# Performance work log

Hardware: AMD Instinct MI355X
Metric: run time of the kernel (lower is better)

## Reference

```python
import jax, jax.numpy as jnp
import numpy as np

HIDDEN = 2048
INTER = 1408
N_ROUTED = 32
N_SHARED = 2
TOP_K = 6
B, S = 2, 1024


def setup_inputs() -> dict:
    key = jax.random.key(0)
    ks = jax.random.split(key, 9)
    scale = 0.02
    x = jax.random.normal(ks[0], (B, S, HIDDEN), dtype=jnp.float32)
    w_router = jax.random.normal(ks[1], (HIDDEN, N_ROUTED), dtype=jnp.float32) * scale
    wg = jax.random.normal(ks[2], (N_ROUTED, HIDDEN, INTER), dtype=jnp.float32) * scale
    wu = jax.random.normal(ks[3], (N_ROUTED, HIDDEN, INTER), dtype=jnp.float32) * scale
    wd = jax.random.normal(ks[4], (N_ROUTED, INTER, HIDDEN), dtype=jnp.float32) * scale
    sg = jax.random.normal(ks[5], (N_SHARED, HIDDEN, INTER), dtype=jnp.float32) * scale
    su = jax.random.normal(ks[6], (N_SHARED, HIDDEN, INTER), dtype=jnp.float32) * scale
    sd = jax.random.normal(ks[7], (N_SHARED, INTER, HIDDEN), dtype=jnp.float32) * scale
    return {"x": x, "w_router": w_router, "wg": wg, "wu": wu, "wd": wd,
            "sg": sg, "su": su, "sd": sd}


def _swiglu(xf, wg_e, wu_e, wd_e):
    # xf: [T, D]; wg_e/wu_e: [D, F]; wd_e: [F, D]
    h = jax.nn.silu(xf @ wg_e) * (xf @ wu_e)
    return h @ wd_e


def reference(x, w_router, wg, wu, wd, sg, su, sd):
    Bb, Ss, D = x.shape
    xf = x.reshape(-1, D)                      # [T, D], T = B*S
    T = xf.shape[0]

    # Shared experts: applied densely to every token, summed.
    shared = jnp.zeros_like(xf)
    for i in range(sg.shape[0]):               # small fixed count (2)
        shared = shared + _swiglu(xf, sg[i], su[i], sd[i])

    # Router: softmax over all routed experts, then top-k + renormalize.
    probs = jax.nn.softmax(xf @ w_router, axis=-1)            # [T, E]
    topw, topi = jax.lax.top_k(probs, TOP_K)                  # [T, K]
    topw = topw / jnp.sum(topw, axis=-1, keepdims=True)

    # Dense [T, E] combine weights (zero where expert not selected).
    E = wg.shape[0]
    wdense = jnp.zeros((T, E), dtype=xf.dtype)
    wdense = wdense.at[jnp.arange(T)[:, None], topi].add(topw)

    # Scan over experts, accumulating weighted expert outputs (memory-light).
    def body(acc, ew):
        wg_e, wu_e, wd_e, w_e = ew            # w_e: [T] combine weight for this expert
        y = _swiglu(xf, wg_e, wu_e, wd_e)     # [T, D]
        return acc + w_e[:, None] * y, None

    routed, _ = jax.lax.scan(body, jnp.zeros_like(xf), (wg, wu, wd, wdense.T))

    return (shared + routed).reshape(Bb, Ss, D)
```

## Files before the change

kernel.cpp:

```cpp
#include <hip/hip_runtime.h>
#include <hip/hip_bf16.h>

#define T_TOK 2048
#define D_HID 2048
#define F_INT 1408
#define N_EXP 32
#define TOPK 6
#define NJOBS 34
#define SH_BASE 12288
#define ROWS_TOTAL 16384
#define MAXT_GU 288
#define MAXT_DN 159
#define LDSW 40

typedef __bf16 bf16;
typedef __bf16 bf16x4 __attribute__((ext_vector_type(4)));
typedef __bf16 bf16x8 __attribute__((ext_vector_type(8)));
typedef float f32x4 __attribute__((ext_vector_type(4)));

#define BAR() asm volatile("s_waitcnt lgkmcnt(0)\n\ts_barrier" ::: "memory")

__device__ __forceinline__ int swz(int r, int k) {
    return r * LDSW + (((k >> 2) ^ ((r >> 2) & 7)) << 2) + (k & 3);
}

__device__ __forceinline__ int decode_tile(const int* __restrict__ counts, int bid,
                                           int NBN, int MSH, int NSH,
                                           int& job, int& n0, int& m0) {
    int total = 0;
    for (int j = 0; j < NJOBS; ++j) {
        int c = (j < N_EXP) ? counts[j] : T_TOK;
        total += ((c + (1 << MSH) - 1) >> MSH) * NBN;
    }
    if (bid >= total) return 0;
    int q = total >> 3, r = total & 7, x = bid & 7, o = bid >> 3;
    int L = (x < r ? x * (q + 1) : r * (q + 1) + (x - r) * q) + o;
    int acc = 0;
    for (int j = 0; j < NJOBS; ++j) {
        int c = (j < N_EXP) ? counts[j] : T_TOK;
        int tc = (c + (1 << MSH) - 1) >> MSH;
        int b = tc * NBN;
        if (L < acc + b) {
            int rem = L - acc;
            int n0i = rem / tc;
            job = j;
            n0 = n0i << NSH;
            m0 = (rem - n0i * tc) << MSH;
            return 1;
        }
        acc += b;
    }
    return 0;
}

__global__ __launch_bounds__(256) void k_router(const float* __restrict__ x,
                                                const float* __restrict__ wr,
                                                int* __restrict__ counts,
                                                int* __restrict__ tok_e,
                                                float* __restrict__ tok_w) {
    int t = blockIdx.x;
    int tid = threadIdx.x;
    __shared__ float xs[D_HID];
    __shared__ float part[8][32];
    __shared__ float probs[N_EXP];

    const float4* xsrc = (const float4*)(x + (size_t)t * D_HID);
    float4* xdst = (float4*)xs;
    for (int i = tid; i < D_HID / 4; i += 256) xdst[i] = xsrc[i];
    __syncthreads();

    int e = tid & 31, c = tid >> 5;
    float p = 0.f;
    const float* wp = wr + e;
    #pragma unroll 8
    for (int h = c * 256; h < c * 256 + 256; ++h) p += xs[h] * wp[h * 32];
    part[c][e] = p;
    __syncthreads();

    if (tid < 32) {
        float l = 0.f;
        #pragma unroll
        for (int cc = 0; cc < 8; ++cc) l += part[cc][tid];
        float m = l;
        for (int off = 16; off; off >>= 1) m = fmaxf(m, __shfl_xor(m, off));
        float ex = __expf(l - m);
        float s = ex;
        for (int off = 16; off; off >>= 1) s += __shfl_xor(s, off);
        probs[tid] = ex / s;
    }
    __syncthreads();

    if (tid == 0) {
        unsigned used = 0;
        int ids[TOPK]; float wsv[TOPK]; float wsum = 0.f;
        for (int k = 0; k < TOPK; ++k) {
            int best = 0; float bv = -1.f;
            for (int ee = 0; ee < N_EXP; ++ee)
                if (!((used >> ee) & 1u) && probs[ee] > bv) { bv = probs[ee]; best = ee; }
            used |= 1u << best;
            ids[k] = best; wsv[k] = bv; wsum += bv;
        }
        float inv = 1.f / wsum;
        for (int k = 0; k < TOPK; ++k) {
            tok_e[t * TOPK + k] = ids[k];
            tok_w[t * TOPK + k] = wsv[k] * inv;
            atomicAdd(&counts[ids[k]], 1);
        }
    }
}

__global__ void k_plan(const int* __restrict__ counts, int* __restrict__ offs,
                       int* __restrict__ cursors) {
    int tid = threadIdx.x;
    if (tid < N_EXP) cursors[tid] = 0;
    if (tid == 0) {
        int o = 0;
        offs[0] = 0;
        for (int e2 = 0; e2 < N_EXP; ++e2) { o += counts[e2]; offs[e2 + 1] = o; }
        offs[33] = offs[32] + T_TOK;
        offs[34] = offs[33] + T_TOK;
    }
}

__global__ __launch_bounds__(256) void k_assign(const int* __restrict__ tok_e,
                                                const int* __restrict__ offs,
                                                int* __restrict__ cursors,
                                                int* __restrict__ slots,
                                                int* __restrict__ rowtok) {
    int t = blockIdx.x * 256 + threadIdx.x;
    #pragma unroll
    for (int k = 0; k < TOPK; ++k) {
        int e = tok_e[t * TOPK + k];
        int pos = atomicAdd(&cursors[e], 1);
        int slot = offs[e] + pos;
        slots[t * TOPK + k] = slot;
        rowtok[slot] = t;
    }
    rowtok[SH_BASE + t] = t;
    rowtok[SH_BASE + T_TOK + t] = t;
}

__global__ __launch_bounds__(256, 3) void k_gateup(
    const float* __restrict__ x, const float* __restrict__ wg, const float* __restrict__ wu,
    const float* __restrict__ sg, const float* __restrict__ su,
    const int* __restrict__ rowtok, const int* __restrict__ counts, const int* __restrict__ offs,
    bf16* __restrict__ H) {

    int job, n0, m0;
    if (!decode_tile(counts, blockIdx.x, F_INT / 128, 6, 7, job, n0, m0)) return;
    int cnt = (job < N_EXP) ? counts[job] : T_TOK;
    int base = offs[job];
    const float* Wg = (job < N_EXP) ? wg + (size_t)job * D_HID * F_INT
                                    : sg + (size_t)(job - N_EXP) * D_HID * F_INT;
    const float* Wu = (job < N_EXP) ? wu + (size_t)job * D_HID * F_INT
                                    : su + (size_t)(job - N_EXP) * D_HID * F_INT;

    __shared__ bf16 As[2][64 * LDSW];
    __shared__ bf16 Bg[2][128 * LDSW];
    __shared__ bf16 Bu[2][128 * LDSW];

    int tid = threadIdx.x;
    int lane = tid & 63;
    int wid = tid >> 6;
    int wm = (wid >> 1) * 32;
    int wn = (wid & 1) * 64;

    int ar = tid >> 2;
    int akh = (tid & 3) * 8;
    int grow_a = m0 + ar; if (grow_a > cnt - 1) grow_a = cnt - 1;
    const float* asrc = x + (size_t)rowtok[base + grow_a] * D_HID + akh;

    int k4 = (tid >> 5) * 4;
    int nn = (tid & 31) * 4;
    const float* gsrc = Wg + (size_t)k4 * F_INT + n0 + nn;
    const float* usrc = Wu + (size_t)k4 * F_INT + n0 + nn;

    f32x4 accg[2][4], accu[2][4];
    f32x4 zero = {0.f, 0.f, 0.f, 0.f};
    #pragma unroll
    for (int i = 0; i < 2; ++i)
        #pragma unroll
        for (int j = 0; j < 4; ++j) { accg[i][j] = zero; accu[i][j] = zero; }

    float4 a_r[2], g_r[4], u_r[4];

    auto LOAD = [&](int k0) {
        const float4* s4 = (const float4*)(asrc + k0);
        a_r[0] = s4[0]; a_r[1] = s4[1];
        const float* g0 = gsrc + (size_t)k0 * F_INT;
        g_r[0] = *(const float4*)g0;
        g_r[1] = *(const float4*)(g0 + F_INT);
        g_r[2] = *(const float4*)(g0 + 2 * F_INT);
        g_r[3] = *(const float4*)(g0 + 3 * F_INT);
        const float* u0 = usrc + (size_t)k0 * F_INT;
        u_r[0] = *(const float4*)u0;
        u_r[1] = *(const float4*)(u0 + F_INT);
        u_r[2] = *(const float4*)(u0 + 2 * F_INT);
        u_r[3] = *(const float4*)(u0 + 3 * F_INT);
    };

    auto WRITE = [&](int s) {
        #pragma unroll
        for (int q = 0; q < 2; ++q) {
            float4 f = a_r[q];
            bf16x4 v = {(bf16)f.x, (bf16)f.y, (bf16)f.z, (bf16)f.w};
            *(bf16x4*)&As[s][swz(ar, akh + 4 * q)] = v;
        }
        bf16x4 p0 = {(bf16)g_r[0].x, (bf16)g_r[1].x, (bf16)g_r[2].x, (bf16)g_r[3].x};
        bf16x4 p1 = {(bf16)g_r[0].y, (bf16)g_r[1].y, (bf16)g_r[2].y, (bf16)g_r[3].y};
        bf16x4 p2 = {(bf16)g_r[0].z, (bf16)g_r[1].z, (bf16)g_r[2].z, (bf16)g_r[3].z};
        bf16x4 p3 = {(bf16)g_r[0].w, (bf16)g_r[1].w, (bf16)g_r[2].w, (bf16)g_r[3].w};
        *(bf16x4*)&Bg[s][swz(nn + 0, k4)] = p0;
        *(bf16x4*)&Bg[s][swz(nn + 1, k4)] = p1;
        *(bf16x4*)&Bg[s][swz(nn + 2, k4)] = p2;
        *(bf16x4*)&Bg[s][swz(nn + 3, k4)] = p3;
        bf16x4 q0 = {(bf16)u_r[0].x, (bf16)u_r[1].x, (bf16)u_r[2].x, (bf16)u_r[3].x};
        bf16x4 q1 = {(bf16)u_r[0].y, (bf16)u_r[1].y, (bf16)u_r[2].y, (bf16)u_r[3].y};
        bf16x4 q2 = {(bf16)u_r[0].z, (bf16)u_r[1].z, (bf16)u_r[2].z, (bf16)u_r[3].z};
        bf16x4 q3 = {(bf16)u_r[0].w, (bf16)u_r[1].w, (bf16)u_r[2].w, (bf16)u_r[3].w};
        *(bf16x4*)&Bu[s][swz(nn + 0, k4)] = q0;
        *(bf16x4*)&Bu[s][swz(nn + 1, k4)] = q1;
        *(bf16x4*)&Bu[s][swz(nn + 2, k4)] = q2;
        *(bf16x4*)&Bu[s][swz(nn + 3, k4)] = q3;
    };

    const int NT = D_HID / 32;
    LOAD(0);
    WRITE(0);
    LOAD(32);
    BAR();

    for (int kt = 0; kt < NT; ++kt) {
        int cur = kt & 1;
        if (kt + 1 < NT) WRITE(cur ^ 1);
        if (kt + 2 < NT) LOAD((kt + 2) * 32);

        int kk = (lane >> 4) * 8;
        bf16x8 af[2];
        #pragma unroll
        for (int mf = 0; mf < 2; ++mf) {
            int R = wm + mf * 16 + (lane & 15);
            bf16x4 lo = *(const bf16x4*)&As[cur][swz(R, kk)];
            bf16x4 hi = *(const bf16x4*)&As[cur][swz(R, kk + 4)];
            af[mf] = __builtin_shufflevector(lo, hi, 0, 1, 2, 3, 4, 5, 6, 7);
        }
        #pragma unroll
        for (int nf = 0; nf < 4; ++nf) {
            int rn = wn + nf * 16 + (lane & 15);
            int o0 = swz(rn, kk), o1 = swz(rn, kk + 4);
            bf16x4 bl = *(const bf16x4*)&Bg[cur][o0];
            bf16x4 bh = *(const bf16x4*)&Bg[cur][o1];
            bf16x8 bfr = __builtin_shufflevector(bl, bh, 0, 1, 2, 3, 4, 5, 6, 7);
            bf16x4 ul = *(const bf16x4*)&Bu[cur][o0];
            bf16x4 uh = *(const bf16x4*)&Bu[cur][o1];
            bf16x8 ufr = __builtin_shufflevector(ul, uh, 0, 1, 2, 3, 4, 5, 6, 7);
            #pragma unroll
            for (int mf = 0; mf < 2; ++mf) {
                accg[mf][nf] = __builtin_amdgcn_mfma_f32_16x16x32_bf16(af[mf], bfr, accg[mf][nf], 0, 0, 0);
                accu[mf][nf] = __builtin_amdgcn_mfma_f32_16x16x32_bf16(af[mf], ufr, accu[mf][nf], 0, 0, 0);
            }
        }
        BAR();
    }

    #pragma unroll
    for (int mf = 0; mf < 2; ++mf) {
        #pragma unroll
        for (int nf = 0; nf < 4; ++nf) {
            int col = n0 + wn + nf * 16 + (lane & 15);
            #pragma unroll
            for (int r = 0; r < 4; ++r) {
                int grow = m0 + wm + mf * 16 + (lane >> 4) * 4 + r;
                if (grow < cnt) {
                    float g = accg[mf][nf][r];
                    float u = accu[mf][nf][r];
                    float h = g * u / (1.f + __expf(-g));
                    H[(size_t)(base + grow) * F_INT + col] = (bf16)h;
                }
            }
        }
    }
}

__global__ __launch_bounds__(256, 3) void k_down(
    const bf16* __restrict__ H, const float* __restrict__ wd, const float* __restrict__ sd,
    const int* __restrict__ counts, const int* __restrict__ offs,
    bf16* __restrict__ P) {

    int job, n0, m0;
    if (!decode_tile(counts, blockIdx.x, D_HID / 128, 7, 7, job, n0, m0)) return;
    int cnt = (job < N_EXP) ? counts[job] : T_TOK;
    int base = offs[job];
    const float* Wd = (job < N_EXP) ? wd + (size_t)job * F_INT * D_HID
                                    : sd + (size_t)(job - N_EXP) * F_INT * D_HID;

    __shared__ bf16 As[2][128 * LDSW];
    __shared__ bf16 Bs[2][128 * LDSW];

    int tid = threadIdx.x;
    int lane = tid & 63;
    int wid = tid >> 6;
    int wm = (wid >> 1) * 64;
    int wn = (wid & 1) * 64;

    int ar = tid >> 1;
    int akh = (tid & 1) * 16;
    int grow_a = m0 + ar; if (grow_a > cnt - 1) grow_a = cnt - 1;
    const bf16* asrc = H + (size_t)(base + grow_a) * F_INT + akh;

    int k4 = (tid >> 5) * 4;
    int nn = (tid & 31) * 4;
    const float* bsrc = Wd + (size_t)k4 * D_HID + n0 + nn;

    f32x4 acc[4][4];
    f32x4 zero = {0.f, 0.f, 0.f, 0.f};
    #pragma unroll
    for (int i = 0; i < 4; ++i)
        #pragma unroll
        for (int j = 0; j < 4; ++j) acc[i][j] = zero;

    bf16x8 h_r[2];
    float4 b_r[4];

    auto LOAD = [&](int k0) {
        h_r[0] = *(const bf16x8*)(asrc + k0);
        h_r[1] = *(const bf16x8*)(asrc + k0 + 8);
        const float* b0 = bsrc + (size_t)k0 * D_HID;
        b_r[0] = *(const float4*)b0;
        b_r[1] = *(const float4*)(b0 + D_HID);
        b_r[2] = *(const float4*)(b0 + 2 * D_HID);
        b_r[3] = *(const float4*)(b0 + 3 * D_HID);
    };

    auto WRITE = [&](int s) {
        bf16x4 w0 = __builtin_shufflevector(h_r[0], h_r[0], 0, 1, 2, 3);
        bf16x4 w1 = __builtin_shufflevector(h_r[0], h_r[0], 4, 5, 6, 7);
        bf16x4 w2 = __builtin_shufflevector(h_r[1], h_r[1], 0, 1, 2, 3);
        bf16x4 w3 = __builtin_shufflevector(h_r[1], h_r[1], 4, 5, 6, 7);
        *(bf16x4*)&As[s][swz(ar, akh + 0)]  = w0;
        *(bf16x4*)&As[s][swz(ar, akh + 4)]  = w1;
        *(bf16x4*)&As[s][swz(ar, akh + 8)]  = w2;
        *(bf16x4*)&As[s][swz(ar, akh + 12)] = w3;
        bf16x4 p0 = {(bf16)b_r[0].x, (bf16)b_r[1].x, (bf16)b_r[2].x, (bf16)b_r[3].x};
        bf16x4 p1 = {(bf16)b_r[0].y, (bf16)b_r[1].y, (bf16)b_r[2].y, (bf16)b_r[3].y};
        bf16x4 p2 = {(bf16)b_r[0].z, (bf16)b_r[1].z, (bf16)b_r[2].z, (bf16)b_r[3].z};
        bf16x4 p3 = {(bf16)b_r[0].w, (bf16)b_r[1].w, (bf16)b_r[2].w, (bf16)b_r[3].w};
        *(bf16x4*)&Bs[s][swz(nn + 0, k4)] = p0;
        *(bf16x4*)&Bs[s][swz(nn + 1, k4)] = p1;
        *(bf16x4*)&Bs[s][swz(nn + 2, k4)] = p2;
        *(bf16x4*)&Bs[s][swz(nn + 3, k4)] = p3;
    };

    const int NT = F_INT / 32;
    LOAD(0);
    WRITE(0);
    LOAD(32);
    BAR();

    for (int kt = 0; kt < NT; ++kt) {
        int cur = kt & 1;
        if (kt + 1 < NT) WRITE(cur ^ 1);
        if (kt + 2 < NT) LOAD((kt + 2) * 32);

        int kk = (lane >> 4) * 8;
        bf16x8 af[4];
        #pragma unroll
        for (int mf = 0; mf < 4; ++mf) {
            int R = wm + mf * 16 + (lane & 15);
            bf16x4 lo = *(const bf16x4*)&As[cur][swz(R, kk)];
            bf16x4 hi = *(const bf16x4*)&As[cur][swz(R, kk + 4)];
            af[mf] = __builtin_shufflevector(lo, hi, 0, 1, 2, 3, 4, 5, 6, 7);
        }
        #pragma unroll
        for (int nf = 0; nf < 4; ++nf) {
            int rn = wn + nf * 16 + (lane & 15);
            bf16x4 bl = *(const bf16x4*)&Bs[cur][swz(rn, kk)];
            bf16x4 bh = *(const bf16x4*)&Bs[cur][swz(rn, kk + 4)];
            bf16x8 bfr = __builtin_shufflevector(bl, bh, 0, 1, 2, 3, 4, 5, 6, 7);
            #pragma unroll
            for (int mf = 0; mf < 4; ++mf)
                acc[mf][nf] = __builtin_amdgcn_mfma_f32_16x16x32_bf16(af[mf], bfr, acc[mf][nf], 0, 0, 0);
        }
        BAR();
    }

    #pragma unroll
    for (int mf = 0; mf < 4; ++mf) {
        #pragma unroll
        for (int nf = 0; nf < 4; ++nf) {
            int col = n0 + wn + nf * 16 + (lane & 15);
            #pragma unroll
            for (int r = 0; r < 4; ++r) {
                int grow = m0 + wm + mf * 16 + (lane >> 4) * 4 + r;
                if (grow < cnt)
                    P[(size_t)(base + grow) * D_HID + col] = (bf16)acc[mf][nf][r];
            }
        }
    }
}

__global__ __launch_bounds__(256) void k_combine(const bf16* __restrict__ P,
                                                 const int* __restrict__ slots,
                                                 const float* __restrict__ tok_w,
                                                 float* __restrict__ out) {
    int t = blockIdx.x;
    int tid = threadIdx.x;
    __shared__ int ss[TOPK];
    __shared__ float ww[TOPK];
    if (tid < TOPK) { ss[tid] = slots[t * TOPK + tid]; ww[tid] = tok_w[t * TOPK + tid]; }
    __syncthreads();
    int c0 = tid * 8;
    float acc[8];
    {
        bf16x8 v0 = *(const bf16x8*)(P + (size_t)(SH_BASE + t) * D_HID + c0);
        bf16x8 v1 = *(const bf16x8*)(P + (size_t)(SH_BASE + T_TOK + t) * D_HID + c0);
        #pragma unroll
        for (int i = 0; i < 8; ++i) acc[i] = (float)v0[i] + (float)v1[i];
    }
    #pragma unroll
    for (int k = 0; k < TOPK; ++k) {
        bf16x8 v = *(const bf16x8*)(P + (size_t)ss[k] * D_HID + c0);
        float w = ww[k];
        #pragma unroll
        for (int i = 0; i < 8; ++i) acc[i] += w * (float)v[i];
    }
    float4 o0 = {acc[0], acc[1], acc[2], acc[3]};
    float4 o1 = {acc[4], acc[5], acc[6], acc[7]};
    *(float4*)(out + (size_t)t * D_HID + c0) = o0;
    *(float4*)(out + (size_t)t * D_HID + c0 + 4) = o1;
}

extern "C" void kernel_launch(void* const* d_in, const int* in_sizes, int n_in,
                              void* d_out, int out_size, void* d_ws, size_t ws_size,
                              hipStream_t stream) {
    const float* x  = (const float*)d_in[0];
    const float* wr = (const float*)d_in[1];
    const float* wg = (const float*)d_in[2];
    const float* wu = (const float*)d_in[3];
    const float* wd = (const float*)d_in[4];
    const float* sg = (const float*)d_in[5];
    const float* su = (const float*)d_in[6];
    const float* sd = (const float*)d_in[7];
    float* out = (float*)d_out;

    char* w = (char*)d_ws;
    int*   counts   = (int*)(w + 0);
    int*   cursors  = (int*)(w + 256);
    int*   offs     = (int*)(w + 512);
    int*   tok_e    = (int*)(w + 8192);
    float* tok_w    = (float*)(w + 8192 + 49152);
    int*   slots    = (int*)(w + 8192 + 2 * 49152);
    int*   rowtok   = (int*)(w + 8192 + 3 * 49152);
    bf16*  H        = (bf16*)(w + 262144);
    bf16*  P        = (bf16*)(w + 262144 + (size_t)ROWS_TOTAL * F_INT * 2);

    hipMemsetAsync(counts, 0, 128, stream);
    k_router<<<T_TOK, 256, 0, stream>>>(x, wr, counts, tok_e, tok_w);
    k_plan<<<1, 64, 0, stream>>>(counts, offs, cursors);
    k_assign<<<T_TOK / 256, 256, 0, stream>>>(tok_e, offs, cursors, slots, rowtok);
    k_gateup<<<MAXT_GU * (F_INT / 128), 256, 0, stream>>>(
        x, wg, wu, sg, su, rowtok, counts, offs, H);
    k_down<<<MAXT_DN * (D_HID / 128), 256, 0, stream>>>(
        H, wd, sd, counts, offs, P);
    k_combine<<<T_TOK, 256, 0, stream>>>(P, slots, tok_w, out);
}
```

Measured before the change: 811.4 us.

## Pre-convert activations to bf16 and use 16-byte LDS swizzle for fragment loads

Adds a kernel that converts x to bf16 once, so the gate/up GEMM gathers half as many activation bytes and skips the per-tile float-to-bf16 conversion. The LDS swizzle moves from 4-element to 8-element granularity, so A and B fragments are read with a single 16-byte LDS load instead of two 8-byte loads and a shuffle. This costs an extra launch plus an extra write and read of the converted activations, and the new swizzle may change bank-conflict behaviour for the 4-element transposed B-tile stores.

```diff
diff --git a/kernel.cpp b/kernel.cpp
--- a/kernel.cpp
+++ b/kernel.cpp
@@ -20,8 +20,8 @@
 
 #define BAR() asm volatile("s_waitcnt lgkmcnt(0)\n\ts_barrier" ::: "memory")
 
-__device__ __forceinline__ int swz(int r, int k) {
-    return r * LDSW + (((k >> 2) ^ ((r >> 2) & 7)) << 2) + (k & 3);
+__device__ __forceinline__ int swz16(int r, int k) {
+    return r * LDSW + (((k >> 3) ^ ((r >> 3) & 3)) << 3) + (k & 7);
 }
 
 __device__ __forceinline__ int decode_tile(const int* __restrict__ counts, int bid,
@@ -53,6 +53,16 @@
     return 0;
 }
 
+__global__ __launch_bounds__(256) void k_xcvt(const float* __restrict__ x,
+                                              bf16* __restrict__ xb) {
+    int i = blockIdx.x * 2048 + threadIdx.x * 8;
+    float4 f0 = *(const float4*)(x + i);
+    float4 f1 = *(const float4*)(x + i + 4);
+    bf16x8 v = {(bf16)f0.x, (bf16)f0.y, (bf16)f0.z, (bf16)f0.w,
+                (bf16)f1.x, (bf16)f1.y, (bf16)f1.z, (bf16)f1.w};
+    *(bf16x8*)(xb + i) = v;
+}
+
 __global__ __launch_bounds__(256) void k_router(const float* __restrict__ x,
                                                 const float* __restrict__ wr,
                                                 int* __restrict__ counts,
@@ -141,7 +151,7 @@
 }
 
 __global__ __launch_bounds__(256, 3) void k_gateup(
-    const float* __restrict__ x, const float* __restrict__ wg, const float* __restrict__ wu,
+    const bf16* __restrict__ xb, const float* __restrict__ wg, const float* __restrict__ wu,
     const float* __restrict__ sg, const float* __restrict__ su,
     const int* __restrict__ rowtok, const int* __restrict__ counts, const int* __restrict__ offs,
     bf16* __restrict__ H) {
@@ -166,9 +176,9 @@
     int wn = (wid & 1) * 64;
 
     int ar = tid >> 2;
-    int akh = (tid & 3) * 8;
+    int akg = tid & 3;
     int grow_a = m0 + ar; if (grow_a > cnt - 1) grow_a = cnt - 1;
-    const float* asrc = x + (size_t)rowtok[base + grow_a] * D_HID + akh;
+    const bf16* asrc = xb + (size_t)rowtok[base + grow_a] * D_HID + akg * 8;
 
     int k4 = (tid >> 5) * 4;
     int nn = (tid & 31) * 4;
@@ -182,11 +192,11 @@
         #pragma unroll
         for (int j = 0; j < 4; ++j) { accg[i][j] = zero; accu[i][j] = zero; }
 
-    float4 a_r[2], g_r[4], u_r[4];
+    bf16x8 a_r8;
+    float4 g_r[4], u_r[4];
 
     auto LOAD = [&](int k0) {
-        const float4* s4 = (const float4*)(asrc + k0);
-        a_r[0] = s4[0]; a_r[1] = s4[1];
+        a_r8 = *(const bf16x8*)(asrc + k0);
         const float* g0 = gsrc + (size_t)k0 * F_INT;
         g_r[0] = *(const float4*)g0;
         g_r[1] = *(const float4*)(g0 + F_INT);
@@ -200,28 +210,23 @@
     };
 
     auto WRITE = [&](int s) {
-        #pragma unroll
-        for (int q = 0; q < 2; ++q) {
-            float4 f = a_r[q];
-            bf16x4 v = {(bf16)f.x, (bf16)f.y, (bf16)f.z, (bf16)f.w};
-            *(bf16x4*)&As[s][swz(ar, akh + 4 * q)] = v;
-        }
+        *(bf16x8*)&As[s][swz16(ar, akg * 8)] = a_r8;
         bf16x4 p0 = {(bf16)g_r[0].x, (bf16)g_r[1].x, (bf16)g_r[2].x, (bf16)g_r[3].x};
         bf16x4 p1 = {(bf16)g_r[0].y, (bf16)g_r[1].y, (bf16)g_r[2].y, (bf16)g_r[3].y};
         bf16x4 p2 = {(bf16)g_r[0].z, (bf16)g_r[1].z, (bf16)g_r[2].z, (bf16)g_r[3].z};
         bf16x4 p3 = {(bf16)g_r[0].w, (bf16)g_r[1].w, (bf16)g_r[2].w, (bf16)g_r[3].w};
-        *(bf16x4*)&Bg[s][swz(nn + 0, k4)] = p0;
-        *(bf16x4*)&Bg[s][swz(nn + 1, k4)] = p1;
-        *(bf16x4*)&Bg[s][swz(nn + 2, k4)] = p2;
-        *(bf16x4*)&Bg[s][swz(nn + 3, k4)] = p3;
+        *(bf16x4*)&Bg[s][swz16(nn + 0, k4)] = p0;
+        *(bf16x4*)&Bg[s][swz16(nn + 1, k4)] = p1;
+        *(bf16x4*)&Bg[s][swz16(nn + 2, k4)] = p2;
+        *(bf16x4*)&Bg[s][swz16(nn + 3, k4)] = p3;
         bf16x4 q0 = {(bf16)u_r[0].x, (bf16)u_r[1].x, (bf16)u_r[2].x, (bf16)u_r[3].x};
         bf16x4 q1 = {(bf16)u_r[0].y, (bf16)u_r[1].y, (bf16)u_r[2].y, (bf16)u_r[3].y};
         bf16x4 q2 = {(bf16)u_r[0].z, (bf16)u_r[1].z, (bf16)u_r[2].z, (bf16)u_r[3].z};
         bf16x4 q3 = {(bf16)u_r[0].w, (bf16)u_r[1].w, (bf16)u_r[2].w, (bf16)u_r[3].w};
-        *(bf16x4*)&Bu[s][swz(nn + 0, k4)] = q0;
-        *(bf16x4*)&Bu[s][swz(nn + 1, k4)] = q1;
-        *(bf16x4*)&Bu[s][swz(nn + 2, k4)] = q2;
-        *(bf16x4*)&Bu[s][swz(nn + 3, k4)] = q3;
+        *(bf16x4*)&Bu[s][swz16(nn + 0, k4)] = q0;
+        *(bf16x4*)&Bu[s][swz16(nn + 1, k4)] = q1;
+        *(bf16x4*)&Bu[s][swz16(nn + 2, k4)] = q2;
+        *(bf16x4*)&Bu[s][swz16(nn + 3, k4)] = q3;
     };
 
     const int NT = D_HID / 32;
@@ -235,25 +240,16 @@
         if (kt + 1 < NT) WRITE(cur ^ 1);
         if (kt + 2 < NT) LOAD((kt + 2) * 32);
 
-        int kk = (lane >> 4) * 8;
+        int kgl = (lane >> 4) * 8;
         bf16x8 af[2];
         #pragma unroll
-        for (int mf = 0; mf < 2; ++mf) {
-            int R = wm + mf * 16 + (lane & 15);
-            bf16x4 lo = *(const bf16x4*)&As[cur][swz(R, kk)];
-            bf16x4 hi = *(const bf16x4*)&As[cur][swz(R, kk + 4)];
-            af[mf] = __builtin_shufflevector(lo, hi, 0, 1, 2, 3, 4, 5, 6, 7);
-        }
+        for (int mf = 0; mf < 2; ++mf)
+            af[mf] = *(const bf16x8*)&As[cur][swz16(wm + mf * 16 + (lane & 15), kgl)];
         #pragma unroll
         for (int nf = 0; nf < 4; ++nf) {
             int rn = wn + nf * 16 + (lane & 15);
-            int o0 = swz(rn, kk), o1 = swz(rn, kk + 4);
-            bf16x4 bl = *(const bf16x4*)&Bg[cur][o0];
-            bf16x4 bh = *(const bf16x4*)&Bg[cur][o1];
-            bf16x8 bfr = __builtin_shufflevector(bl, bh, 0, 1, 2, 3, 4, 5, 6, 7);
-            bf16x4 ul = *(const bf16x4*)&Bu[cur][o0];
-            bf16x4 uh = *(const bf16x4*)&Bu[cur][o1];
-            bf16x8 ufr = __builtin_shufflevector(ul, uh, 0, 1, 2, 3, 4, 5, 6, 7);
+            bf16x8 bfr = *(const bf16x8*)&Bg[cur][swz16(rn, kgl)];
+            bf16x8 ufr = *(const bf16x8*)&Bu[cur][swz16(rn, kgl)];
             #pragma unroll
             for (int mf = 0; mf < 2; ++mf) {
                 accg[mf][nf] = __builtin_amdgcn_mfma_f32_16x16x32_bf16(af[mf], bfr, accg[mf][nf], 0, 0, 0);
@@ -304,9 +300,9 @@
     int wn = (wid & 1) * 64;
 
     int ar = tid >> 1;
-    int akh = (tid & 1) * 16;
+    int akg2 = (tid & 1) * 2;
     int grow_a = m0 + ar; if (grow_a > cnt - 1) grow_a = cnt - 1;
-    const bf16* asrc = H + (size_t)(base + grow_a) * F_INT + akh;
+    const bf16* asrc = H + (size_t)(base + grow_a) * F_INT + akg2 * 8;
 
     int k4 = (tid >> 5) * 4;
     int nn = (tid & 31) * 4;
@@ -333,22 +329,16 @@
     };
 
     auto WRITE = [&](int s) {
-        bf16x4 w0 = __builtin_shufflevector(h_r[0], h_r[0], 0, 1, 2, 3);
-        bf16x4 w1 = __builtin_shufflevector(h_r[0], h_r[0], 4, 5, 6, 7);
-        bf16x4 w2 = __builtin_shufflevector(h_r[1], h_r[1], 0, 1, 2, 3);
-        bf16x4 w3 = __builtin_shufflevector(h_r[1], h_r[1], 4, 5, 6, 7);
-        *(bf16x4*)&As[s][swz(ar, akh + 0)]  = w0;
-        *(bf16x4*)&As[s][swz(ar, akh + 4)]  = w1;
-        *(bf16x4*)&As[s][swz(ar, akh + 8)]  = w2;
-        *(bf16x4*)&As[s][swz(ar, akh + 12)] = w3;
+        *(bf16x8*)&As[s][swz16(ar, akg2 * 8)] = h_r[0];
+        *(bf16x8*)&As[s][swz16(ar, (akg2 + 1) * 8)] = h_r[1];
         bf16x4 p0 = {(bf16)b_r[0].x, (bf16)b_r[1].x, (bf16)b_r[2].x, (bf16)b_r[3].x};
         bf16x4 p1 = {(bf16)b_r[0].y, (bf16)b_r[1].y, (bf16)b_r[2].y, (bf16)b_r[3].y};
         bf16x4 p2 = {(bf16)b_r[0].z, (bf16)b_r[1].z, (bf16)b_r[2].z, (bf16)b_r[3].z};
         bf16x4 p3 = {(bf16)b_r[0].w, (bf16)b_r[1].w, (bf16)b_r[2].w, (bf16)b_r[3].w};
-        *(bf16x4*)&Bs[s][swz(nn + 0, k4)] = p0;
-        *(bf16x4*)&Bs[s][swz(nn + 1, k4)] = p1;
-        *(bf16x4*)&Bs[s][swz(nn + 2, k4)] = p2;
-        *(bf16x4*)&Bs[s][swz(nn + 3, k4)] = p3;
+        *(bf16x4*)&Bs[s][swz16(nn + 0, k4)] = p0;
+        *(bf16x4*)&Bs[s][swz16(nn + 1, k4)] = p1;
+        *(bf16x4*)&Bs[s][swz16(nn + 2, k4)] = p2;
+        *(bf16x4*)&Bs[s][swz16(nn + 3, k4)] = p3;
     };
 
     const int NT = F_INT / 32;
@@ -362,21 +352,15 @@
         if (kt + 1 < NT) WRITE(cur ^ 1);
         if (kt + 2 < NT) LOAD((kt + 2) * 32);
 
-        int kk = (lane >> 4) * 8;
+        int kgl = (lane >> 4) * 8;
         bf16x8 af[4];
         #pragma unroll
-        for (int mf = 0; mf < 4; ++mf) {
-            int R = wm + mf * 16 + (lane & 15);
-            bf16x4 lo = *(const bf16x4*)&As[cur][swz(R, kk)];
-            bf16x4 hi = *(const bf16x4*)&As[cur][swz(R, kk + 4)];
-            af[mf] = __builtin_shufflevector(lo, hi, 0, 1, 2, 3, 4, 5, 6, 7);
-        }
+        for (int mf = 0; mf < 4; ++mf)
+            af[mf] = *(const bf16x8*)&As[cur][swz16(wm + mf * 16 + (lane & 15), kgl)];
         #pragma unroll
         for (int nf = 0; nf < 4; ++nf) {
             int rn = wn + nf * 16 + (lane & 15);
-            bf16x4 bl = *(const bf16x4*)&Bs[cur][swz(rn, kk)];
-            bf16x4 bh = *(const bf16x4*)&Bs[cur][swz(rn, kk + 4)];
-            bf16x8 bfr = __builtin_shufflevector(bl, bh, 0, 1, 2, 3, 4, 5, 6, 7);
+            bf16x8 bfr = *(const bf16x8*)&Bs[cur][swz16(rn, kgl)];
             #pragma unroll
             for (int mf = 0; mf < 4; ++mf)
                 acc[mf][nf] = __builtin_amdgcn_mfma_f32_16x16x32_bf16(af[mf], bfr, acc[mf][nf], 0, 0, 0);
@@ -453,13 +437,16 @@
     int*   rowtok   = (int*)(w + 8192 + 3 * 49152);
     bf16*  H        = (bf16*)(w + 262144);
     bf16*  P        = (bf16*)(w + 262144 + (size_t)ROWS_TOTAL * F_INT * 2);
+    bf16*  Xb       = (bf16*)(w + 262144 + (size_t)ROWS_TOTAL * F_INT * 2
+                                        + (size_t)ROWS_TOTAL * D_HID * 2);
 
     hipMemsetAsync(counts, 0, 128, stream);
+    k_xcvt<<<T_TOK * D_HID / 2048, 256, 0, stream>>>(x, Xb);
     k_router<<<T_TOK, 256, 0, stream>>>(x, wr, counts, tok_e, tok_w);
     k_plan<<<1, 64, 0, stream>>>(counts, offs, cursors);
     k_assign<<<T_TOK / 256, 256, 0, stream>>>(tok_e, offs, cursors, slots, rowtok);
     k_gateup<<<MAXT_GU * (F_INT / 128), 256, 0, stream>>>(
-        x, wg, wu, sg, su, rowtok, counts, offs, H);
+        Xb, wg, wu, sg, su, rowtok, counts, offs, H);
     k_down<<<MAXT_DN * (D_HID / 128), 256, 0, stream>>>(
         H, wd, sd, counts, offs, P);
     k_combine<<<T_TOK, 256, 0, stream>>>(P, slots, tok_w, out);
```

Result: faster. 777.1 us (-4.2%).
